# Kernel optimization log

Measured on AMD Instinct MI355X. Metric: run time of the kernel, lower is better.

The kernel has to match this reference:

```python
import jax, jax.numpy as jnp
import numpy as np

H = 16
D_HEAD = 64  # model_dim // head_count = 1024 // 16
MODEL_DIM = 1024
MODEL_DIM1 = 768


def setup_inputs() -> dict:
    key = jax.random.key(0)
    ks = jax.random.split(key, 12)
    B, Q, K = 4, 1024, 1024
    inp = {
        "key": jax.random.normal(ks[0], (B, K, MODEL_DIM), jnp.float32),
        "value": jax.random.normal(ks[1], (B, K, MODEL_DIM), jnp.float32),
        "query": jax.random.normal(ks[2], (B, Q, MODEL_DIM1), jnp.float32),
        "mask": jax.random.randint(ks[3], (B, Q), 0, 2, jnp.int32),
        "additional_mask": jax.random.randint(ks[4], (B, K), 0, 2, jnp.int32),
        # learned params (nn.Linear weights stored as [in, out] for x @ W)
        "Wk": 0.02 * jax.random.normal(ks[5], (MODEL_DIM, H * D_HEAD), jnp.float32),
        "bk": jnp.zeros((H * D_HEAD,), jnp.float32),
        "Wv": 0.02 * jax.random.normal(ks[6], (MODEL_DIM, H * D_HEAD), jnp.float32),
        "bv": jnp.zeros((H * D_HEAD,), jnp.float32),
        "Wq": 0.02 * jax.random.normal(ks[7], (MODEL_DIM1, H * D_HEAD), jnp.float32),
        "bq": jnp.zeros((H * D_HEAD,), jnp.float32),
        "Wo": 0.02 * jax.random.normal(ks[8], (H * D_HEAD, MODEL_DIM1), jnp.float32),
        "bo": jnp.zeros((MODEL_DIM1,), jnp.float32),
    }
    return inp


def reference(key, value, query, mask, additional_mask, Wk, bk, Wv, bv, Wq, bq, Wo, bo):
    B, K_len = key.shape[0], key.shape[1]
    Q_len = query.shape[1]

    def shape(x):  # [B, L, H*d] -> [B, H, L, d]
        return x.reshape(B, -1, H, D_HEAD).transpose(0, 2, 1, 3)

    k = shape(key @ Wk + bk)
    v = shape(value @ Wv + bv)
    q = shape(query @ Wq + bq) / jnp.sqrt(jnp.float32(D_HEAD))

    scores = jnp.einsum("bhqd,bhkd->bhqk", q, k)  # [B,H,Q,K]
    top_score = scores[:, 0, :, :]  # pre-mask scores of head 0

    neg = jnp.float32(-1e18)
    scores = jnp.where(mask[:, None, :, None] == 0, neg, scores)
    scores = jnp.where(additional_mask[:, None, None, :] == 0, neg, scores)

    attn = jax.nn.softmax(scores, axis=-1)
    # dropout omitted (eval mode / deterministic reference)
    ctx = jnp.einsum("bhqk,bhkd->bhqd", attn, v)
    ctx = ctx.transpose(0, 2, 1, 3).reshape(B, Q_len, H * D_HEAD)
    output = ctx @ Wo + bo
    return output, top_score
```

## Files before the change

kernel.cpp:

```cpp
#include <hip/hip_runtime.h>
#include <hip/hip_bf16.h>

typedef __bf16 bf16_t;
typedef __bf16 bf16x8 __attribute__((ext_vector_type(8)));
typedef __bf16 bf16x4 __attribute__((ext_vector_type(4)));
typedef float  f32x4  __attribute__((ext_vector_type(4)));
typedef int    i32x4  __attribute__((ext_vector_type(4)));

#define MFMA16(a,b,c) __builtin_amdgcn_mfma_f32_16x16x32_bf16((a),(b),(c),0,0,0)

static constexpr int Bn = 4, Hn = 16, Dh = 64, SEQ = 1024;

__device__ __forceinline__ void gll16(const void* g, void* l) {
    __builtin_amdgcn_global_load_lds(
        (const __attribute__((address_space(1))) void*)g,
        (__attribute__((address_space(3))) void*)l, 16, 0, 0);
}

__global__ __launch_bounds__(256)
void wtrans_kernel(const float* __restrict__ s0, const float* __restrict__ s1,
                   const float* __restrict__ s2, const float* __restrict__ s3,
                   bf16_t* __restrict__ d0, bf16_t* __restrict__ d1,
                   bf16_t* __restrict__ d2, bf16_t* __restrict__ d3)
{
    __shared__ bf16_t tile[64][72];
    const int bid = blockIdx.x, t = threadIdx.x;
    const float* src; bf16_t* dst; int R, C, tr, tc;
    if (bid < 256)      { src = s0; dst = d0; R = 1024; C = 1024; tr = bid >> 4;        tc = bid & 15; }
    else if (bid < 512) { src = s1; dst = d1; R = 1024; C = 1024; tr = (bid-256) >> 4;  tc = (bid-256) & 15; }
    else if (bid < 704) { src = s2; dst = d2; R = 768;  C = 1024; tr = (bid-512) >> 4;  tc = (bid-512) & 15; }
    else                { src = s3; dst = d3; R = 1024; C = 768;  tr = (bid-704) / 12;  tc = (bid-704) % 12; }
    const int r0 = tr * 64, c0 = tc * 64;
    const int lr = t >> 2, lc0 = (t & 3) * 16;
    #pragma unroll
    for (int i = 0; i < 4; i++) {
        f32x4 v = *(const f32x4*)&src[(size_t)(r0 + lr) * C + c0 + lc0 + i * 4];
        #pragma unroll
        for (int j = 0; j < 4; j++) tile[lr][lc0 + i * 4 + j] = (bf16_t)v[j];
    }
    __syncthreads();
    const int oc = t >> 2, orc0 = (t & 3) * 16;
    #pragma unroll
    for (int i = 0; i < 2; i++) {
        bf16x8 vv;
        #pragma unroll
        for (int j = 0; j < 8; j++) vv[j] = tile[orc0 + i * 8 + j][oc];
        *(bf16x8*)&dst[(size_t)(c0 + oc) * R + r0 + orc0 + i * 8] = vv;
    }
}

template<int KD, int N, int MODE, typename AT>
__global__ __launch_bounds__(256)
void gemm_bt(const AT* __restrict__ A, const bf16_t* __restrict__ Bt,
             const float* __restrict__ bias, void* __restrict__ outp,
             float scale)
{
    __shared__ bf16_t As[2][128 * 64];
    __shared__ bf16_t Bs[2][64 * 64];
    __shared__ bf16_t Ct[(MODE == 2) ? 1 : 128 * 72];
    const int t = threadIdx.x, lane = t & 63, w = t >> 6;
    const int wr = w >> 1, wc = w & 1;
    const int row0 = blockIdx.y * 128, col0 = blockIdx.x * 64;
    const int lrow = lane & 15, lk4 = lane >> 4, lk8 = lk4 * 8;
    const int ar = t >> 1, ac0 = (t & 1) * 32;

    f32x4 acc[4][2] = {};
    f32x4 a_f[8];

    auto aload = [&](int kk) {
        if constexpr (sizeof(AT) == 4) {
            const float* src = (const float*)A + (size_t)(row0 + ar) * KD + kk + ac0;
            #pragma unroll
            for (int j = 0; j < 8; j++) a_f[j] = *(const f32x4*)(src + j * 4);
        }
    };
    auto awrite = [&](int buf) {
        if constexpr (sizeof(AT) == 4) {
            char* base = (char*)&As[buf][0] + ar * 128;
            const int aswz = (ar & 7) << 4;
            #pragma unroll
            for (int j = 0; j < 4; j++) {
                bf16x8 v;
                #pragma unroll
                for (int e = 0; e < 4; e++) {
                    v[e]     = (bf16_t)a_f[2 * j][e];
                    v[4 + e] = (bf16_t)a_f[2 * j + 1][e];
                }
                *(bf16x8*)(base + ((ac0 * 2 + j * 16) ^ aswz)) = v;
            }
        }
    };
    auto astage_gll = [&](int buf, int kk) {
        if constexpr (sizeof(AT) == 2) {
            #pragma unroll
            for (int j = 0; j < 4; j++) {
                const int idx = j * 256 + t;
                const int row = idx >> 3, colb = (idx & 7) * 16;
                const bf16_t* g = (const bf16_t*)A + (size_t)(row0 + row) * KD +
                                  kk + ((colb ^ ((row & 7) << 4)) >> 1);
                gll16(g, (char*)&As[buf][0] + (j * 256 + w * 64) * 16);
            }
        }
    };
    auto bstage = [&](int buf, int kk) {
        #pragma unroll
        for (int j = 0; j < 2; j++) {
            const int idx = j * 256 + t;
            const int n = idx >> 3, colb = (idx & 7) * 16;
            const bf16_t* g = Bt + (size_t)(col0 + n) * KD +
                              kk + ((colb ^ ((n & 7) << 4)) >> 1);
            gll16(g, (char*)&Bs[buf][0] + (j * 256 + w * 64) * 16);
        }
    };

    constexpr int NB = KD / 64;
    if constexpr (sizeof(AT) == 4) { aload(0); awrite(0); }
    else                            astage_gll(0, 0);
    bstage(0, 0);

    const char* AsC0 = (const char*)&As[0][0];
    const char* BsC0 = (const char*)&Bs[0][0];
    for (int s = 0; s < NB; s++) {
        __syncthreads();
        const int cur = s & 1;
        if (s + 1 < NB) {
            bstage(cur ^ 1, (s + 1) * 64);
            if constexpr (sizeof(AT) == 4) aload((s + 1) * 64);
            else                           astage_gll(cur ^ 1, (s + 1) * 64);
        }
        const char* AsC = AsC0 + cur * (128 * 128);
        const char* BsC = BsC0 + cur * (64 * 128);
        #pragma unroll
        for (int h = 0; h < 2; h++) {
            bf16x8 af[4], bfr[2];
            #pragma unroll
            for (int mf = 0; mf < 4; mf++) {
                const int R = wr * 64 + mf * 16 + lrow;
                af[mf] = *(const bf16x8*)(AsC + R * 128 +
                          (((h * 32 + lk8) * 2) ^ ((R & 7) << 4)));
            }
            #pragma unroll
            for (int nf = 0; nf < 2; nf++) {
                const int Rn = wc * 32 + nf * 16 + lrow;
                bfr[nf] = *(const bf16x8*)(BsC + Rn * 128 +
                          (((h * 32 + lk8) * 2) ^ ((Rn & 7) << 4)));
            }
            #pragma unroll
            for (int mf = 0; mf < 4; mf++)
                #pragma unroll
                for (int nf = 0; nf < 2; nf++)
                    acc[mf][nf] = MFMA16(af[mf], bfr[nf], acc[mf][nf]);
        }
        if (s + 1 < NB) { if constexpr (sizeof(AT) == 4) awrite(cur ^ 1); }
    }

    if constexpr (MODE == 2) {
        #pragma unroll
        for (int mf = 0; mf < 4; mf++)
            #pragma unroll
            for (int nf = 0; nf < 2; nf++) {
                const int gcol = col0 + wc * 32 + nf * 16 + lrow;
                const float bv = bias[gcol];
                #pragma unroll
                for (int r = 0; r < 4; r++) {
                    const int grow = row0 + wr * 64 + mf * 16 + lk4 * 4 + r;
                    ((float*)outp)[(size_t)grow * N + gcol] = (acc[mf][nf][r] + bv) * scale;
                }
            }
    } else {
        __syncthreads();
        #pragma unroll
        for (int mf = 0; mf < 4; mf++)
            #pragma unroll
            for (int nf = 0; nf < 2; nf++) {
                const int lcol = wc * 32 + nf * 16 + lrow;
                const float bv = bias[col0 + lcol];
                #pragma unroll
                for (int r = 0; r < 4; r++)
                    Ct[(wr * 64 + mf * 16 + lk4 * 4 + r) * 72 + lcol] =
                        (bf16_t)((acc[mf][nf][r] + bv) * scale);
            }
        __syncthreads();
        const int h = col0 >> 6, b = row0 >> 10;
        bf16_t* op = (bf16_t*)outp + ((size_t)(b * Hn + h) << 16);
        if constexpr (MODE == 0) {
            #pragma unroll
            for (int j = 0; j < 4; j++) {
                const int sl = j * 32 + (t >> 3), cl0 = (t & 7) * 8;
                bf16x8 v = *(const bf16x8*)&Ct[sl * 72 + cl0];
                *(bf16x8*)&op[(size_t)((row0 & 1023) + sl) * 64 + cl0] = v;
            }
        } else {
            #pragma unroll
            for (int jj = 0; jj < 2; jj++) {
                const int cl = jj * 32 + (t >> 3);
                #pragma unroll
                for (int k = 0; k < 2; k++) {
                    const int sl0 = k * 64 + (t & 7) * 8;
                    bf16x8 v;
                    #pragma unroll
                    for (int i = 0; i < 8; i++) v[i] = Ct[(sl0 + i) * 72 + cl];
                    *(bf16x8*)&op[(size_t)cl * 1024 + (row0 & 1023) + sl0] = v;
                }
            }
        }
    }
}

__global__ __launch_bounds__(256)
void attn_kernel(const bf16_t* __restrict__ kbuf, const bf16_t* __restrict__ vT,
                 const bf16_t* __restrict__ qbuf, const int* __restrict__ qmask,
                 const int* __restrict__ kmask, bf16_t* __restrict__ ctx)
{
    __shared__ bf16_t Pall[4][16 * 64];
    const int t = threadIdx.x, lane = t & 63, w = t >> 6;
    const int bidx = blockIdx.x;
    const int qt = bidx & 15, bh = bidx >> 4, b = bh >> 4, h = bh & 15;
    const int lrow = lane & 15, lk4 = lane >> 4, lk8 = lk4 * 8;
    const int wrow0 = qt * 64 + w * 16;
    const bf16_t* kb = kbuf + (size_t)bh * SEQ * Dh;
    const bf16_t* vb = vT + (size_t)bh * Dh * SEQ;
    char* Pw = (char*)&Pall[w][0];
    const int sw = (lrow & 7) << 4;

    bf16x8 aq0, aq1;
    {
        const bf16_t* qp = qbuf + ((size_t)bh * SEQ + wrow0 + lrow) * Dh + lk8;
        aq0 = *(const bf16x8*)(qp);
        aq1 = *(const bf16x8*)(qp + 32);
    }
    const int qm = qmask[b * SEQ + wrow0 + lrow];

    bf16x8 ones;
    #pragma unroll
    for (int i = 0; i < 8; i++) ones[i] = (bf16_t)1.0f;

    float m_run = -__builtin_inff();
    f32x4 o[4] = {};
    f32x4 o_l  = {};

    bf16x8 kc0[4], kc1[4];
    #pragma unroll
    for (int nf = 0; nf < 4; nf++) {
        const bf16_t* kp = kb + (size_t)(nf * 16 + lrow) * Dh + lk8;
        kc0[nf] = *(const bf16x8*)(kp);
        kc1[nf] = *(const bf16x8*)(kp + 32);
    }

    for (int kt = 0; kt < 16; kt++) {
        const int key0 = kt * 64;
        bf16x8 vf0[4], vf1[4];
        #pragma unroll
        for (int nf = 0; nf < 4; nf++) {
            const bf16_t* vp = vb + (size_t)(nf * 16 + lrow) * SEQ + key0 + lk8;
            vf0[nf] = *(const bf16x8*)(vp);
            vf1[nf] = *(const bf16x8*)(vp + 32);
        }
        i32x4 km[4];
        #pragma unroll
        for (int nf = 0; nf < 4; nf++)
            km[nf] = *(const i32x4*)&kmask[b * SEQ + key0 + nf * 16 + lk4 * 4];
        f32x4 s4[4] = {};
        __builtin_amdgcn_s_setprio(1);
        #pragma unroll
        for (int nf = 0; nf < 4; nf++) {
            s4[nf] = MFMA16(kc0[nf], aq0, s4[nf]);
            s4[nf] = MFMA16(kc1[nf], aq1, s4[nf]);
        }
        __builtin_amdgcn_s_setprio(0);
        bf16x8 kn0[4], kn1[4];
        if (kt < 15) {
            #pragma unroll
            for (int nf = 0; nf < 4; nf++) {
                const bf16_t* kp = kb + (size_t)(key0 + 64 + nf * 16 + lrow) * Dh + lk8;
                kn0[nf] = *(const bf16x8*)(kp);
                kn1[nf] = *(const bf16x8*)(kp + 32);
            }
        }
        float p[4][4], mx[4];
        #pragma unroll
        for (int nf = 0; nf < 4; nf++) {
            #pragma unroll
            for (int r = 0; r < 4; r++)
                p[nf][r] = (qm && km[nf][r]) ? s4[nf][r] : -1e18f;
            mx[nf] = fmaxf(fmaxf(p[nf][0], p[nf][1]), fmaxf(p[nf][2], p[nf][3]));
        }
        const float pmax = fmaxf(fmaxf(mx[0], mx[1]), fmaxf(mx[2], mx[3]));
        if (!__all(pmax - m_run <= 8.0f)) {
            float mt = fmaxf(pmax, __shfl_xor(pmax, 16));
            mt = fmaxf(mt, __shfl_xor(mt, 32));
            const float resc = __expf(m_run - mt);
            m_run = mt;
            #pragma unroll
            for (int nf = 0; nf < 4; nf++)
                #pragma unroll
                for (int r = 0; r < 4; r++) o[nf][r] *= resc;
            #pragma unroll
            for (int r = 0; r < 4; r++) o_l[r] *= resc;
        }
        #pragma unroll
        for (int nf = 0; nf < 4; nf++)
            #pragma unroll
            for (int r = 0; r < 4; r++) p[nf][r] = __expf(p[nf][r] - m_run);
        #pragma unroll
        for (int nf = 0; nf < 4; nf++) {
            bf16x4 pk;
            #pragma unroll
            for (int r = 0; r < 4; r++) pk[r] = (bf16_t)p[nf][r];
            *(bf16x4*)(Pw + lrow * 128 + ((nf * 32 + lk4 * 8) ^ sw)) = pk;
        }
        bf16x8 pa0 = *(const bf16x8*)(Pw + lrow * 128 + ((lk4 * 16) ^ sw));
        bf16x8 pa1 = *(const bf16x8*)(Pw + lrow * 128 + ((64 + lk4 * 16) ^ sw));
        __builtin_amdgcn_s_setprio(1);
        #pragma unroll
        for (int nf = 0; nf < 4; nf++) {
            o[nf] = MFMA16(vf0[nf], pa0, o[nf]);
            o[nf] = MFMA16(vf1[nf], pa1, o[nf]);
        }
        o_l = MFMA16(ones, pa0, o_l);
        o_l = MFMA16(ones, pa1, o_l);
        __builtin_amdgcn_s_setprio(0);
        #pragma unroll
        for (int nf = 0; nf < 4; nf++) { kc0[nf] = kn0[nf]; kc1[nf] = kn1[nf]; }
    }
    const float inv = 1.0f / o_l[0];
    #pragma unroll
    for (int nf = 0; nf < 4; nf++) {
        bf16x4 pk;
        #pragma unroll
        for (int r = 0; r < 4; r++) pk[r] = (bf16_t)(o[nf][r] * inv);
        *(bf16x4*)(Pw + lrow * 128 + ((nf * 32 + lk4 * 8) ^ sw)) = pk;
    }
    const int qp2 = lane >> 2, ch = lane & 3;
    const int sw2 = (qp2 & 7) << 4;
    bf16x8 o0 = *(const bf16x8*)(Pw + qp2 * 128 + ((ch * 32) ^ sw2));
    bf16x8 o1 = *(const bf16x8*)(Pw + qp2 * 128 + ((ch * 32 + 16) ^ sw2));
    bf16_t* cp = ctx + ((size_t)(b * SEQ + wrow0 + qp2)) * 1024 + h * 64 + ch * 16;
    *(bf16x8*)cp = o0;
    *(bf16x8*)(cp + 8) = o1;
}

__global__ __launch_bounds__(256)
void topsc_kernel(const bf16_t* __restrict__ kbuf, const bf16_t* __restrict__ qbuf,
                  float* __restrict__ topsc)
{
    const int t = threadIdx.x, lane = t & 63, w = t >> 6;
    const int bx = blockIdx.x;
    const int b = bx >> 6, qt = (bx >> 2) & 15, kq = bx & 3;
    const int lrow = lane & 15, lk4 = lane >> 4, lk8 = lk4 * 8;
    const int wrow0 = qt * 64 + w * 16;
    const bf16_t* kb = kbuf + ((size_t)(b * Hn)) * SEQ * Dh;
    const bf16_t* qp = qbuf + ((size_t)(b * Hn)) * SEQ * Dh
                     + (size_t)(wrow0 + lrow) * Dh + lk8;
    bf16x8 aq0 = *(const bf16x8*)(qp);
    bf16x8 aq1 = *(const bf16x8*)(qp + 32);
    for (int kt = 0; kt < 4; kt++) {
        const int key0 = kq * 256 + kt * 64;
        f32x4 s4[4] = {};
        #pragma unroll
        for (int nf = 0; nf < 4; nf++) {
            const bf16_t* kp = kb + (size_t)(key0 + nf * 16 + lrow) * Dh + lk8;
            s4[nf] = MFMA16(aq0, *(const bf16x8*)(kp), s4[nf]);
            s4[nf] = MFMA16(aq1, *(const bf16x8*)(kp + 32), s4[nf]);
        }
        #pragma unroll
        for (int nf = 0; nf < 4; nf++)
            #pragma unroll
            for (int r = 0; r < 4; r++)
                topsc[(size_t)(b * SEQ + wrow0 + lk4 * 4 + r) * SEQ +
                      key0 + nf * 16 + lrow] = s4[nf][r];
    }
}

extern "C" void kernel_launch(void* const* d_in, const int* in_sizes, int n_in,
                              void* d_out, int out_size, void* d_ws, size_t ws_size,
                              hipStream_t stream)
{
    const float* key   = (const float*)d_in[0];
    const float* value = (const float*)d_in[1];
    const float* query = (const float*)d_in[2];
    const int*   mask  = (const int*)d_in[3];
    const int*   amask = (const int*)d_in[4];
    const float* Wk = (const float*)d_in[5];
    const float* bk = (const float*)d_in[6];
    const float* Wv = (const float*)d_in[7];
    const float* bv = (const float*)d_in[8];
    const float* Wq = (const float*)d_in[9];
    const float* bq = (const float*)d_in[10];
    const float* Wo = (const float*)d_in[11];
    const float* bo = (const float*)d_in[12];

    const size_t per = (size_t)Bn * Hn * SEQ * Dh;
    bf16_t* kproj = (bf16_t*)d_ws;
    bf16_t* vT    = kproj + per;
    bf16_t* qproj = vT + per;
    bf16_t* ctx   = qproj + per;

    float* outf = (float*)d_out;
    bf16_t* WkT = (bf16_t*)(outf + (size_t)Bn * SEQ * 768);
    bf16_t* WvT = WkT + 1024 * 1024;
    bf16_t* WqT = WvT + 1024 * 1024;
    bf16_t* WoT = WqT + 1024 * 768;
    float* topsc = outf + (size_t)Bn * SEQ * 768;

    wtrans_kernel<<<896, 256, 0, stream>>>(Wk, Wv, Wq, Wo, WkT, WvT, WqT, WoT);
    gemm_bt<1024, 1024, 0, float><<<dim3(16, 32), 256, 0, stream>>>(key,   WkT, bk, kproj, 1.0f);
    gemm_bt<1024, 1024, 1, float><<<dim3(16, 32), 256, 0, stream>>>(value, WvT, bv, vT,    1.0f);
    gemm_bt< 768, 1024, 0, float><<<dim3(16, 32), 256, 0, stream>>>(query, WqT, bq, qproj, 0.125f);
    attn_kernel<<<dim3(Bn * Hn * 16), 256, 0, stream>>>(kproj, vT, qproj, mask, amask, ctx);
    gemm_bt<1024, 768, 2, bf16_t><<<dim3(12, 32), 256, 0, stream>>>(ctx, WoT, bo, outf, 1.0f);
    topsc_kernel<<<256, 256, 0, stream>>>(kproj, qproj, topsc);
}
```

Baseline: 382.9 us.

## Shrink GEMM tiles to 64x64, add XCD-aware block remapping, split topsc wider

The projection GEMMs move from 128x64 to 64x64 tiles and reuse the A shared buffer as the epilogue staging area, which doubles the block count and cuts LDS use per block. GEMM and attention blocks are remapped with an XCD-aware swizzle so neighbouring row tiles or heads run on the same chiplet and share L2. The topsc kernel is split into 4x more blocks, each handling one 64-key tile. Smaller tiles lower arithmetic intensity and increase global reads of the weights, in exchange for better occupancy and CU coverage.

```diff
diff --git a/kernel.cpp b/kernel.cpp
--- a/kernel.cpp
+++ b/kernel.cpp
@@ -23,7 +23,7 @@
                    bf16_t* __restrict__ d0, bf16_t* __restrict__ d1,
                    bf16_t* __restrict__ d2, bf16_t* __restrict__ d3)
 {
-    __shared__ bf16_t tile[64][72];
+    __shared__ bf16_t tile[64][68];
     const int bid = blockIdx.x, t = threadIdx.x;
     const float* src; bf16_t* dst; int R, C, tr, tc;
     if (bid < 256)      { src = s0; dst = d0; R = 1024; C = 1024; tr = bid >> 4;        tc = bid & 15; }
@@ -49,29 +49,32 @@
     }
 }
 
-template<int KD, int N, int MODE, typename AT>
+template<int KD, int N, int MODE, int GX, typename AT>
 __global__ __launch_bounds__(256)
 void gemm_bt(const AT* __restrict__ A, const bf16_t* __restrict__ Bt,
              const float* __restrict__ bias, void* __restrict__ outp,
              float scale)
 {
-    __shared__ bf16_t As[2][128 * 64];
+    __shared__ bf16_t As[2][64 * 64];
     __shared__ bf16_t Bs[2][64 * 64];
-    __shared__ bf16_t Ct[(MODE == 2) ? 1 : 128 * 72];
+    bf16_t* Ct = &As[0][0];
     const int t = threadIdx.x, lane = t & 63, w = t >> 6;
     const int wr = w >> 1, wc = w & 1;
-    const int row0 = blockIdx.y * 128, col0 = blockIdx.x * 64;
+    const int bidx = blockIdx.x;
+    const int xcd = bidx & 7, slot = bidx >> 3;
+    const int row0 = (xcd + 8 * (slot / GX)) * 64;
+    const int col0 = (slot % GX) * 64;
     const int lrow = lane & 15, lk4 = lane >> 4, lk8 = lk4 * 8;
-    const int ar = t >> 1, ac0 = (t & 1) * 32;
-
-    f32x4 acc[4][2] = {};
-    f32x4 a_f[8];
+    const int ar = t >> 2, ac0 = (t & 3) * 16;
+
+    f32x4 acc[2][2] = {};
+    f32x4 a_f[4];
 
     auto aload = [&](int kk) {
         if constexpr (sizeof(AT) == 4) {
             const float* src = (const float*)A + (size_t)(row0 + ar) * KD + kk + ac0;
             #pragma unroll
-            for (int j = 0; j < 8; j++) a_f[j] = *(const f32x4*)(src + j * 4);
+            for (int j = 0; j < 4; j++) a_f[j] = *(const f32x4*)(src + j * 4);
         }
     };
     auto awrite = [&](int buf) {
@@ -79,7 +82,7 @@
             char* base = (char*)&As[buf][0] + ar * 128;
             const int aswz = (ar & 7) << 4;
             #pragma unroll
-            for (int j = 0; j < 4; j++) {
+            for (int j = 0; j < 2; j++) {
                 bf16x8 v;
                 #pragma unroll
                 for (int e = 0; e < 4; e++) {
@@ -93,7 +96,7 @@
     auto astage_gll = [&](int buf, int kk) {
         if constexpr (sizeof(AT) == 2) {
             #pragma unroll
-            for (int j = 0; j < 4; j++) {
+            for (int j = 0; j < 2; j++) {
                 const int idx = j * 256 + t;
                 const int row = idx >> 3, colb = (idx & 7) * 16;
                 const bf16_t* g = (const bf16_t*)A + (size_t)(row0 + row) * KD +
@@ -128,14 +131,14 @@
             if constexpr (sizeof(AT) == 4) aload((s + 1) * 64);
             else                           astage_gll(cur ^ 1, (s + 1) * 64);
         }
-        const char* AsC = AsC0 + cur * (128 * 128);
+        const char* AsC = AsC0 + cur * (64 * 128);
         const char* BsC = BsC0 + cur * (64 * 128);
         #pragma unroll
         for (int h = 0; h < 2; h++) {
-            bf16x8 af[4], bfr[2];
-            #pragma unroll
-            for (int mf = 0; mf < 4; mf++) {
-                const int R = wr * 64 + mf * 16 + lrow;
+            bf16x8 af[2], bfr[2];
+            #pragma unroll
+            for (int mf = 0; mf < 2; mf++) {
+                const int R = wr * 32 + mf * 16 + lrow;
                 af[mf] = *(const bf16x8*)(AsC + R * 128 +
                           (((h * 32 + lk8) * 2) ^ ((R & 7) << 4)));
             }
@@ -146,7 +149,7 @@
                           (((h * 32 + lk8) * 2) ^ ((Rn & 7) << 4)));
             }
             #pragma unroll
-            for (int mf = 0; mf < 4; mf++)
+            for (int mf = 0; mf < 2; mf++)
                 #pragma unroll
                 for (int nf = 0; nf < 2; nf++)
                     acc[mf][nf] = MFMA16(af[mf], bfr[nf], acc[mf][nf]);
@@ -156,28 +159,28 @@
 
     if constexpr (MODE == 2) {
         #pragma unroll
-        for (int mf = 0; mf < 4; mf++)
+        for (int mf = 0; mf < 2; mf++)
             #pragma unroll
             for (int nf = 0; nf < 2; nf++) {
                 const int gcol = col0 + wc * 32 + nf * 16 + lrow;
                 const float bv = bias[gcol];
                 #pragma unroll
                 for (int r = 0; r < 4; r++) {
-                    const int grow = row0 + wr * 64 + mf * 16 + lk4 * 4 + r;
+                    const int grow = row0 + wr * 32 + mf * 16 + lk4 * 4 + r;
                     ((float*)outp)[(size_t)grow * N + gcol] = (acc[mf][nf][r] + bv) * scale;
                 }
             }
     } else {
         __syncthreads();
         #pragma unroll
-        for (int mf = 0; mf < 4; mf++)
+        for (int mf = 0; mf < 2; mf++)
             #pragma unroll
             for (int nf = 0; nf < 2; nf++) {
                 const int lcol = wc * 32 + nf * 16 + lrow;
                 const float bv = bias[col0 + lcol];
                 #pragma unroll
                 for (int r = 0; r < 4; r++)
-                    Ct[(wr * 64 + mf * 16 + lk4 * 4 + r) * 72 + lcol] =
+                    Ct[(wr * 32 + mf * 16 + lk4 * 4 + r) * 72 + lcol] =
                         (bf16_t)((acc[mf][nf][r] + bv) * scale);
             }
         __syncthreads();
@@ -185,7 +188,7 @@
         bf16_t* op = (bf16_t*)outp + ((size_t)(b * Hn + h) << 16);
         if constexpr (MODE == 0) {
             #pragma unroll
-            for (int j = 0; j < 4; j++) {
+            for (int j = 0; j < 2; j++) {
                 const int sl = j * 32 + (t >> 3), cl0 = (t & 7) * 8;
                 bf16x8 v = *(const bf16x8*)&Ct[sl * 72 + cl0];
                 *(bf16x8*)&op[(size_t)((row0 & 1023) + sl) * 64 + cl0] = v;
@@ -194,14 +197,11 @@
             #pragma unroll
             for (int jj = 0; jj < 2; jj++) {
                 const int cl = jj * 32 + (t >> 3);
-                #pragma unroll
-                for (int k = 0; k < 2; k++) {
-                    const int sl0 = k * 64 + (t & 7) * 8;
-                    bf16x8 v;
-                    #pragma unroll
-                    for (int i = 0; i < 8; i++) v[i] = Ct[(sl0 + i) * 72 + cl];
-                    *(bf16x8*)&op[(size_t)cl * 1024 + (row0 & 1023) + sl0] = v;
-                }
+                const int sl0 = (t & 7) * 8;
+                bf16x8 v;
+                #pragma unroll
+                for (int i = 0; i < 8; i++) v[i] = Ct[(sl0 + i) * 72 + cl];
+                *(bf16x8*)&op[(size_t)cl * 1024 + (row0 & 1023) + sl0] = v;
             }
         }
     }
@@ -215,7 +215,9 @@
     __shared__ bf16_t Pall[4][16 * 64];
     const int t = threadIdx.x, lane = t & 63, w = t >> 6;
     const int bidx = blockIdx.x;
-    const int qt = bidx & 15, bh = bidx >> 4, b = bh >> 4, h = bh & 15;
+    const int xcd = bidx & 7, slot = bidx >> 3;
+    const int qt = slot & 15, bh = xcd + ((slot >> 4) << 3);
+    const int b = bh >> 4, h = bh & 15;
     const int lrow = lane & 15, lk4 = lane >> 4, lk8 = lk4 * 8;
     const int wrow0 = qt * 64 + w * 16;
     const bf16_t* kb = kbuf + (size_t)bh * SEQ * Dh;
@@ -346,7 +348,7 @@
 {
     const int t = threadIdx.x, lane = t & 63, w = t >> 6;
     const int bx = blockIdx.x;
-    const int b = bx >> 6, qt = (bx >> 2) & 15, kq = bx & 3;
+    const int b = bx >> 8, qt = (bx >> 4) & 15, kq = bx & 15;
     const int lrow = lane & 15, lk4 = lane >> 4, lk8 = lk4 * 8;
     const int wrow0 = qt * 64 + w * 16;
     const bf16_t* kb = kbuf + ((size_t)(b * Hn)) * SEQ * Dh;
@@ -354,22 +356,20 @@
                      + (size_t)(wrow0 + lrow) * Dh + lk8;
     bf16x8 aq0 = *(const bf16x8*)(qp);
     bf16x8 aq1 = *(const bf16x8*)(qp + 32);
-    for (int kt = 0; kt < 4; kt++) {
-        const int key0 = kq * 256 + kt * 64;
-        f32x4 s4[4] = {};
-        #pragma unroll
-        for (int nf = 0; nf < 4; nf++) {
-            const bf16_t* kp = kb + (size_t)(key0 + nf * 16 + lrow) * Dh + lk8;
-            s4[nf] = MFMA16(aq0, *(const bf16x8*)(kp), s4[nf]);
-            s4[nf] = MFMA16(aq1, *(const bf16x8*)(kp + 32), s4[nf]);
-        }
-        #pragma unroll
-        for (int nf = 0; nf < 4; nf++)
-            #pragma unroll
-            for (int r = 0; r < 4; r++)
-                topsc[(size_t)(b * SEQ + wrow0 + lk4 * 4 + r) * SEQ +
-                      key0 + nf * 16 + lrow] = s4[nf][r];
-    }
+    const int key0 = kq * 64;
+    f32x4 s4[4] = {};
+    #pragma unroll
+    for (int nf = 0; nf < 4; nf++) {
+        const bf16_t* kp = kb + (size_t)(key0 + nf * 16 + lrow) * Dh + lk8;
+        s4[nf] = MFMA16(aq0, *(const bf16x8*)(kp), s4[nf]);
+        s4[nf] = MFMA16(aq1, *(const bf16x8*)(kp + 32), s4[nf]);
+    }
+    #pragma unroll
+    for (int nf = 0; nf < 4; nf++)
+        #pragma unroll
+        for (int r = 0; r < 4; r++)
+            topsc[(size_t)(b * SEQ + wrow0 + lk4 * 4 + r) * SEQ +
+                  key0 + nf * 16 + lrow] = s4[nf][r];
 }
 
 extern "C" void kernel_launch(void* const* d_in, const int* in_sizes, int n_in,
@@ -404,10 +404,10 @@
     float* topsc = outf + (size_t)Bn * SEQ * 768;
 
     wtrans_kernel<<<896, 256, 0, stream>>>(Wk, Wv, Wq, Wo, WkT, WvT, WqT, WoT);
-    gemm_bt<1024, 1024, 0, float><<<dim3(16, 32), 256, 0, stream>>>(key,   WkT, bk, kproj, 1.0f);
-    gemm_bt<1024, 1024, 1, float><<<dim3(16, 32), 256, 0, stream>>>(value, WvT, bv, vT,    1.0f);
-    gemm_bt< 768, 1024, 0, float><<<dim3(16, 32), 256, 0, stream>>>(query, WqT, bq, qproj, 0.125f);
-    attn_kernel<<<dim3(Bn * Hn * 16), 256, 0, stream>>>(kproj, vT, qproj, mask, amask, ctx);
-    gemm_bt<1024, 768, 2, bf16_t><<<dim3(12, 32), 256, 0, stream>>>(ctx, WoT, bo, outf, 1.0f);
-    topsc_kernel<<<256, 256, 0, stream>>>(kproj, qproj, topsc);
-}
+    gemm_bt<1024, 1024, 0, 16, float><<<1024, 256, 0, stream>>>(key,   WkT, bk, kproj, 1.0f);
+    gemm_bt<1024, 1024, 1, 16, float><<<1024, 256, 0, stream>>>(value, WvT, bv, vT,    1.0f);
+    gemm_bt< 768, 1024, 0, 16, float><<<1024, 256, 0, stream>>>(query, WqT, bq, qproj, 0.125f);
+    attn_kernel<<<1024, 256, 0, stream>>>(kproj, vT, qproj, mask, amask, ctx);
+    gemm_bt<1024, 768, 2, 12, bf16_t><<<768, 256, 0, stream>>>(ctx, WoT, bo, outf, 1.0f);
+    topsc_kernel<<<1024, 256, 0, stream>>>(kproj, qproj, topsc);
+}
```

Result: faster. 339.7 us (-11.3%).
